# Kernel optimization log

Measured on AMD Instinct MI355X. Metric: run time of the kernel, lower is better.

## Reference

```python
import jax, jax.numpy as jnp
import numpy as np
from jax import lax

B, L = 4, 512
D_MODEL, D_STATE, D_CONV, EXPAND = 1024, 16, 4, 2
D_INNER = EXPAND * D_MODEL
DT_RANK = (D_MODEL + 15) // 16  # math.ceil(d_model / 16) = 64


def setup_inputs() -> dict:
    key = jax.random.key(0)
    ks = jax.random.split(key, 16)

    def rn(k, shape, scale=1.0):
        return jax.random.normal(k, shape, jnp.float32) * scale

    # A initialized as log(1..d_state) broadcast over d_inner, as in the module
    A_log = jnp.log(jnp.broadcast_to(jnp.arange(1, D_STATE + 1, dtype=jnp.float32), (D_INNER, D_STATE)))
    return {
        "hidden_states": rn(ks[0], (B, L, D_MODEL)),
        "in_proj_w": rn(ks[1], (2 * D_INNER, D_MODEL), D_MODEL ** -0.5),
        "conv1d_w": rn(ks[2], (D_INNER, 1, D_CONV), D_CONV ** -0.5),
        "conv1d_bias": rn(ks[3], (D_INNER,), 0.02),
        "x_proj_w": rn(ks[4], (DT_RANK + 2 * D_STATE, D_INNER), D_INNER ** -0.5),
        "dt_proj_w": rn(ks[5], (D_INNER, DT_RANK), DT_RANK ** -0.5),
        "dt_proj_bias": rn(ks[6], (D_INNER,), 0.02) - 4.0,
        "A_log": A_log,
        "D": jnp.ones((D_INNER,), jnp.float32),
        "conv1d_b_w": rn(ks[7], (D_INNER, 1, D_CONV), D_CONV ** -0.5),
        "conv1d_b_bias": rn(ks[8], (D_INNER,), 0.02),
        "x_proj_b_w": rn(ks[9], (DT_RANK + 2 * D_STATE, D_INNER), D_INNER ** -0.5),
        "dt_proj_b_w": rn(ks[10], (D_INNER, DT_RANK), DT_RANK ** -0.5),
        "dt_proj_b_bias": rn(ks[11], (D_INNER,), 0.02) - 4.0,
        "A_b_log": A_log,
        "D_b": jnp.ones((D_INNER,), jnp.float32),
        "out_proj_w": rn(ks[12], (D_MODEL, D_INNER), D_INNER ** -0.5),
    }


def _selective_scan(u, delta, A, Bm, Cm, Dv):
    # u, delta: [b,l,d]; Bm, Cm: [b,l,n]; A: [d,n]; Dv: [d]
    # h_t = exp(delta_t * A) * h_{t-1} + delta_t * B_t * u_t ; y_t = <h_t, C_t> + D * u_t
    def step(h, inp):
        u_t, dt_t, B_t, C_t = inp  # [b,d], [b,d], [b,n], [b,n]
        dA = jnp.exp(dt_t[:, :, None] * A)  # [b,d,n]
        h = dA * h + (dt_t * u_t)[:, :, None] * B_t[:, None, :]
        y = jnp.einsum('bdn,bn->bd', h, C_t)
        return h, y

    b, l, d = u.shape
    h0 = jnp.zeros((b, d, A.shape[1]), u.dtype)
    xs = (u.transpose(1, 0, 2), delta.transpose(1, 0, 2), Bm.transpose(1, 0, 2), Cm.transpose(1, 0, 2))
    _, ys = lax.scan(step, h0, xs)  # ys: [l,b,d]
    return ys.transpose(1, 0, 2) + u * Dv


def _direction(x_bdl, conv_w, conv_b, xproj_w, dtproj_w, dtproj_b, A_log, Dv):
    # x_bdl: [b, d_inner, l]. torch pads both sides with d_conv-1 then slices [:L] -> causal depthwise conv.
    xc = lax.conv_general_dilated(x_bdl, conv_w, (1,), [(D_CONV - 1, 0)],
                                  dimension_numbers=('NCH', 'OIH', 'NCH'),
                                  feature_group_count=D_INNER)
    xc = (xc + conv_b[None, :, None]).transpose(0, 2, 1)  # [b,l,d_inner]
    x_dbl = xc @ xproj_w.T  # [b,l,dt_rank+2n]
    dt = x_dbl[..., :DT_RANK] @ dtproj_w.T + dtproj_b
    Bm = x_dbl[..., DT_RANK:DT_RANK + D_STATE]
    Cm = x_dbl[..., DT_RANK + D_STATE:]
    xc = jnp.clip(xc, -10.0, 10.0)
    dt = jnp.clip(dt, 1e-5, 1.0)
    # source passes dt_proj.bias again as delta_bias with delta_softplus=True (bias added twice; faithful)
    delta = jax.nn.softplus(dt + dtproj_b)
    A = -jnp.exp(A_log)
    return _selective_scan(xc, delta, A, Bm, Cm, Dv)


def reference(hidden_states, in_proj_w, conv1d_w, conv1d_bias, x_proj_w, dt_proj_w, dt_proj_bias,
              A_log, D, conv1d_b_w, conv1d_b_bias, x_proj_b_w, dt_proj_b_w, dt_proj_b_bias,
              A_b_log, D_b, out_proj_w):
    xz = (hidden_states @ in_proj_w.T).transpose(0, 2, 1)  # [b, 2*d_inner, l]
    x, z = jnp.split(xz, 2, axis=1)  # each [b, d_inner, l]
    y_fwd = _direction(x, conv1d_w, conv1d_bias, x_proj_w, dt_proj_w, dt_proj_bias, A_log, D)
    y_bwd = _direction(x[:, :, ::-1], conv1d_b_w, conv1d_b_bias, x_proj_b_w, dt_proj_b_w,
                       dt_proj_b_bias, A_b_log, D_b)[:, ::-1, :]  # flip back along seq
    y = (y_fwd + y_bwd) * jax.nn.silu(z.transpose(0, 2, 1))  # [b,l,d_inner]
    out = y @ out_proj_w.T  # [b,l,d_model]
    return jnp.nan_to_num(out, nan=0.0, posinf=1.0, neginf=-1.0)
```

## Files before the change

### kernel.cpp

```cpp
#include <hip/hip_runtime.h>
#include <hip/hip_bf16.h>
#include <math.h>

#define BB 4
#define LL 512
#define DMODEL 1024
#define DSTATE 16
#define DCONV 4
#define DINNER 2048
#define DTRANK 64
#define MROWS (BB*LL)
#define G2KS 4
#define SCHUNK 32
#define SNC (LL / SCHUNK)

typedef __hip_bfloat16 bf16;
typedef __attribute__((ext_vector_type(8))) short short8;
typedef __attribute__((ext_vector_type(4))) short short4v;
typedef __attribute__((ext_vector_type(4))) float f32x4;

__device__ __forceinline__ float softplusf(float x) {
    return x > 20.f ? x : log1pf(__expf(x));
}

__device__ __forceinline__ void stage16(const void* g, void* l) {
    __builtin_amdgcn_global_load_lds(
        (const __attribute__((address_space(1))) void*)g,
        (__attribute__((address_space(3))) void*)l, 16, 0, 0);
}

__device__ __forceinline__ bool a_is_arange(const float* Aa) {
    bool ok = true;
#pragma unroll
    for (int n = 1; n < DSTATE; ++n) {
        float k = (float)(n + 1);
        ok = ok && (fabsf(Aa[n] - k * Aa[0]) <= 1e-4f * k * fabsf(Aa[0]));
    }
    return ok;
}

template<int EPI>
__global__ __launch_bounds__(256) void gemm_bf16(
    const bf16* __restrict__ A, const bf16* __restrict__ W,
    float* __restrict__ C, int N, int K, int lda, int ldw, int ldc)
{
    __shared__ bf16 lA[128 * 32];
    __shared__ bf16 lW[128 * 32];

    const int tid = threadIdx.x;
    const int lane = tid & 63;
    const int wid = tid >> 6;
    const int wr = wid >> 1;
    const int wc = wid & 1;
    const int rowBase = blockIdx.y * 128;
    const int colBase = blockIdx.x * 128;

    const int r16 = lane & 15;
    const int kg = lane >> 4;
    const int srow = (lane >> 2);
    const int scol = (lane & 3) * 8;

    f32x4 acc[4][4];
#pragma unroll
    for (int m = 0; m < 4; ++m)
#pragma unroll
        for (int n = 0; n < 4; ++n) acc[m][n] = (f32x4)0.f;

    for (int k0 = 0; k0 < K; k0 += 32) {
#pragma unroll
        for (int c = 0; c < 2; ++c) {
            int r = wid * 32 + c * 16 + srow;
            stage16(&A[(size_t)(rowBase + r) * lda + k0 + scol],
                    &lA[(wid * 32 + c * 16) * 32]);
            stage16(&W[(size_t)(colBase + r) * ldw + k0 + scol],
                    &lW[(wid * 32 + c * 16) * 32]);
        }
        __syncthreads();

        short8 a[4], b[4];
#pragma unroll
        for (int m = 0; m < 4; ++m)
            a[m] = *(const short8*)&lA[(wr * 64 + m * 16 + r16) * 32 + kg * 8];
#pragma unroll
        for (int n = 0; n < 4; ++n)
            b[n] = *(const short8*)&lW[(wc * 64 + n * 16 + r16) * 32 + kg * 8];
#pragma unroll
        for (int m = 0; m < 4; ++m)
#pragma unroll
            for (int n = 0; n < 4; ++n)
                acc[m][n] = __builtin_amdgcn_mfma_f32_16x16x32_bf16(
                    a[m], b[n], acc[m][n], 0, 0, 0);
        __syncthreads();
    }

#pragma unroll
    for (int m = 0; m < 4; ++m) {
#pragma unroll
        for (int n = 0; n < 4; ++n) {
            int gc = colBase + wc * 64 + n * 16 + r16;
#pragma unroll
            for (int j = 0; j < 4; ++j) {
                int gr = rowBase + wr * 64 + m * 16 + kg * 4 + j;
                float v = acc[m][n][j];
                if (EPI == 2) {
                    if (isnan(v)) v = 0.f;
                    else if (isinf(v)) v = (v > 0.f) ? 1.f : -1.f;
                }
                C[(size_t)gr * ldc + gc] = v;
            }
        }
    }
}

__global__ __launch_bounds__(256) void g4_mfma(
    const bf16* __restrict__ A, const bf16* __restrict__ W,
    float* __restrict__ part)
{
    const int kz = blockIdx.z;
    const int kOff = kz * 1024;
    float* C = part + (size_t)kz * 2048 * 1024;

    __shared__ bf16 lA[128 * 32];
    __shared__ bf16 lW[128 * 32];

    const int tid = threadIdx.x;
    const int lane = tid & 63;
    const int wid = tid >> 6;
    const int wr = wid >> 1;
    const int wc = wid & 1;
    const int rowBase = blockIdx.y * 128;
    const int colBase = blockIdx.x * 128;

    const int r16 = lane & 15;
    const int kg = lane >> 4;
    const int srow = (lane >> 2);
    const int scol = (lane & 3) * 8;

    f32x4 acc[4][4];
#pragma unroll
    for (int m = 0; m < 4; ++m)
#pragma unroll
        for (int n = 0; n < 4; ++n) acc[m][n] = (f32x4)0.f;

    for (int k0 = 0; k0 < 1024; k0 += 32) {
#pragma unroll
        for (int c = 0; c < 2; ++c) {
            int r = wid * 32 + c * 16 + srow;
            stage16(&A[(size_t)(rowBase + r) * 2048 + kOff + k0 + scol],
                    &lA[(wid * 32 + c * 16) * 32]);
            stage16(&W[(size_t)(colBase + r) * 2048 + kOff + k0 + scol],
                    &lW[(wid * 32 + c * 16) * 32]);
        }
        __syncthreads();

        short8 a[4], b[4];
#pragma unroll
        for (int m = 0; m < 4; ++m)
            a[m] = *(const short8*)&lA[(wr * 64 + m * 16 + r16) * 32 + kg * 8];
#pragma unroll
        for (int n = 0; n < 4; ++n)
            b[n] = *(const short8*)&lW[(wc * 64 + n * 16 + r16) * 32 + kg * 8];
#pragma unroll
        for (int m = 0; m < 4; ++m)
#pragma unroll
            for (int n = 0; n < 4; ++n)
                acc[m][n] = __builtin_amdgcn_mfma_f32_16x16x32_bf16(
                    a[m], b[n], acc[m][n], 0, 0, 0);
        __syncthreads();
    }

#pragma unroll
    for (int m = 0; m < 4; ++m) {
#pragma unroll
        for (int n = 0; n < 4; ++n) {
            int gc = colBase + wc * 64 + n * 16 + r16;
#pragma unroll
            for (int j = 0; j < 4; ++j) {
                int gr = rowBase + wr * 64 + m * 16 + kg * 4 + j;
                C[(size_t)gr * 1024 + gc] = acc[m][n][j];
            }
        }
    }
}

__global__ __launch_bounds__(256) void g4_reduce(
    const float* __restrict__ part, float* __restrict__ out)
{
    int i = (blockIdx.x * 256 + threadIdx.x) * 4;
    float4 p0 = *(const float4*)&part[i];
    float4 p1 = *(const float4*)&part[2048 * 1024 + i];
    float r[4] = { p0.x + p1.x, p0.y + p1.y, p0.z + p1.z, p0.w + p1.w };
#pragma unroll
    for (int j = 0; j < 4; ++j) {
        float v = r[j];
        if (isnan(v)) v = 0.f;
        else if (isinf(v)) v = (v > 0.f) ? 1.f : -1.f;
        r[j] = v;
    }
    *(float4*)&out[i] = *(float4*)r;
}

__global__ __launch_bounds__(256) void g3_mfma(
    const bf16* __restrict__ xdbl_bf,
    const bf16* __restrict__ dtw_bf,
    const float* __restrict__ biasf, const float* __restrict__ biasb,
    bf16* __restrict__ of, bf16* __restrict__ ob)
{
    const int dir = blockIdx.z;
    const bf16* A = xdbl_bf + (size_t)dir * 2048 * 96;
    const bf16* W = dtw_bf + (size_t)dir * 2048 * 64;
    const float* bias = dir ? biasb : biasf;
    bf16* C = dir ? ob : of;

    __shared__ bf16 lA[128 * 32];
    __shared__ bf16 lW[128 * 32];

    const int tid = threadIdx.x;
    const int lane = tid & 63;
    const int wid = tid >> 6;
    const int wr = wid >> 1;
    const int wc = wid & 1;
    const int rowBase = blockIdx.y * 128;
    const int colBase = blockIdx.x * 128;

    const int r16 = lane & 15;
    const int kg = lane >> 4;
    const int srow = (lane >> 2);
    const int scol = (lane & 3) * 8;

    f32x4 acc[4][4];
#pragma unroll
    for (int m = 0; m < 4; ++m)
#pragma unroll
        for (int n = 0; n < 4; ++n) acc[m][n] = (f32x4)0.f;

#pragma unroll
    for (int k0 = 0; k0 < 64; k0 += 32) {
#pragma unroll
        for (int c = 0; c < 2; ++c) {
            int r = wid * 32 + c * 16 + srow;
            stage16(&A[(size_t)(rowBase + r) * 96 + k0 + scol],
                    &lA[(wid * 32 + c * 16) * 32]);
            stage16(&W[(size_t)(colBase + r) * 64 + k0 + scol],
                    &lW[(wid * 32 + c * 16) * 32]);
        }
        __syncthreads();

        short8 a[4], b[4];
#pragma unroll
        for (int m = 0; m < 4; ++m)
            a[m] = *(const short8*)&lA[(wr * 64 + m * 16 + r16) * 32 + kg * 8];
#pragma unroll
        for (int n = 0; n < 4; ++n)
            b[n] = *(const short8*)&lW[(wc * 64 + n * 16 + r16) * 32 + kg * 8];
#pragma unroll
        for (int m = 0; m < 4; ++m)
#pragma unroll
            for (int n = 0; n < 4; ++n)
                acc[m][n] = __builtin_amdgcn_mfma_f32_16x16x32_bf16(
                    a[m], b[n], acc[m][n], 0, 0, 0);
        __syncthreads();
    }

#pragma unroll
    for (int m = 0; m < 4; ++m) {
#pragma unroll
        for (int n = 0; n < 4; ++n) {
            int gc = colBase + wc * 64 + n * 16 + r16;
            float bv = bias[gc];
#pragma unroll
            for (int j = 0; j < 4; ++j) {
                int gr = rowBase + wr * 64 + m * 16 + kg * 4 + j;
                float t = acc[m][n][j] + bv;
                t = fminf(fmaxf(t, 1e-5f), 1.0f);
                C[(size_t)gr * 2048 + gc] = __float2bfloat16(softplusf(t + bv));
            }
        }
    }
}

__global__ __launch_bounds__(256) void g2_mfma(
    const bf16* __restrict__ xcbf_f, const bf16* __restrict__ xcbf_b,
    const bf16* __restrict__ wxf, const bf16* __restrict__ wxb,
    float* __restrict__ part)
{
    const int dir = blockIdx.z;
    const bf16* A = dir ? xcbf_b : xcbf_f;
    const bf16* W = dir ? wxb : wxf;
    const int rowBase = blockIdx.x * 128;
    const int kz = blockIdx.y;
    const int kBase = kz * (2048 / G2KS);

    __shared__ bf16 lA[128 * 40];
    __shared__ bf16 lW[96 * 40];

    const int tid = threadIdx.x;
    const int lane = tid & 63;
    const int wid = tid >> 6;
    const int r16 = lane & 15;
    const int kg = lane >> 4;

    f32x4 acc[2][6];
#pragma unroll
    for (int m = 0; m < 2; ++m)
#pragma unroll
        for (int n = 0; n < 6; ++n) acc[m][n] = (f32x4)0.f;

    const int srow = tid >> 2;
    const int scol = (tid & 3) * 8;

    for (int k0 = 0; k0 < 2048 / G2KS; k0 += 32) {
#pragma unroll
        for (int it = 0; it < 2; ++it) {
            int r = srow + it * 64;
            short8 va = *(const short8*)&A[(size_t)(rowBase + r) * 2048 + kBase + k0 + scol];
            *(short8*)&lA[r * 40 + scol] = va;
        }
        {
            short8 vw = *(const short8*)&W[(size_t)srow * 2048 + kBase + k0 + scol];
            *(short8*)&lW[srow * 40 + scol] = vw;
        }
        if (tid < 128) {
            int r = 64 + (tid >> 2);
            short8 vw2 = *(const short8*)&W[(size_t)r * 2048 + kBase + k0 + scol];
            *(short8*)&lW[r * 40 + scol] = vw2;
        }
        __syncthreads();

        short8 a[2], b[6];
#pragma unroll
        for (int m = 0; m < 2; ++m)
            a[m] = *(const short8*)&lA[(wid * 32 + m * 16 + r16) * 40 + kg * 8];
#pragma unroll
        for (int n = 0; n < 6; ++n)
            b[n] = *(const short8*)&lW[(n * 16 + r16) * 40 + kg * 8];
#pragma unroll
        for (int m = 0; m < 2; ++m)
#pragma unroll
            for (int n = 0; n < 6; ++n)
                acc[m][n] = __builtin_amdgcn_mfma_f32_16x16x32_bf16(
                    a[m], b[n], acc[m][n], 0, 0, 0);
        __syncthreads();
    }

    float* p = part + ((size_t)(dir * G2KS + kz) * 2048) * 96;
#pragma unroll
    for (int m = 0; m < 2; ++m) {
#pragma unroll
        for (int n = 0; n < 6; ++n) {
            int gc = n * 16 + r16;
#pragma unroll
            for (int j = 0; j < 4; ++j) {
                int gr = rowBase + wid * 32 + m * 16 + kg * 4 + j;
                p[(size_t)gr * 96 + gc] = acc[m][n][j];
            }
        }
    }
}

__global__ __launch_bounds__(256) void g2_reduce(
    const float* __restrict__ part, float* __restrict__ xf, float* __restrict__ xb,
    bf16* __restrict__ xdbl_bf)
{
    int idx = blockIdx.x * 256 + threadIdx.x;
    int c = idx % 96;
    int r = (idx / 96) & 2047;
    int dir = idx / (96 * 2048);
    float s = 0.f;
#pragma unroll
    for (int ks = 0; ks < G2KS; ++ks)
        s += part[((size_t)(dir * G2KS + ks) * 2048 + r) * 96 + c];
    (dir ? xb : xf)[(size_t)r * 96 + c] = s;
    xdbl_bf[((size_t)dir * 2048 + r) * 96 + c] = __float2bfloat16(s);
}

__global__ __launch_bounds__(256) void cast_all(
    const float* __restrict__ hidden, const float* __restrict__ in_proj_w,
    const float* __restrict__ xproj_w, const float* __restrict__ xproj_bw,
    const float* __restrict__ dtproj_w, const float* __restrict__ dtproj_bw,
    bf16* __restrict__ hbf, bf16* __restrict__ wbf,
    bf16* __restrict__ wxf, bf16* __restrict__ wxb,
    bf16* __restrict__ dtwf, bf16* __restrict__ dtwb)
{
    int bid = blockIdx.x;
    const float* src; bf16* dst; int base;
    if (bid < 1024)      { src = hidden;    dst = hbf;  base = bid; }
    else if (bid < 3072) { src = in_proj_w; dst = wbf;  base = bid - 1024; }
    else if (bid < 3168) { src = xproj_w;   dst = wxf;  base = bid - 3072; }
    else if (bid < 3264) { src = xproj_bw;  dst = wxb;  base = bid - 3168; }
    else if (bid < 3328) { src = dtproj_w;  dst = dtwf; base = bid - 3264; }
    else                 { src = dtproj_bw; dst = dtwb; base = bid - 3328; }
    int i = (base * 256 + threadIdx.x) * 8;
    float4 x = *(const float4*)&src[i];
    float4 y = *(const float4*)&src[i + 4];
    bf16 t[8] = { __float2bfloat16(x.x), __float2bfloat16(x.y),
                  __float2bfloat16(x.z), __float2bfloat16(x.w),
                  __float2bfloat16(y.x), __float2bfloat16(y.y),
                  __float2bfloat16(y.z), __float2bfloat16(y.w) };
    *(short8*)&dst[i] = *(short8*)t;
}

__global__ __launch_bounds__(256) void conv_kernel(
    const float* __restrict__ xz,
    const float* __restrict__ wf, const float* __restrict__ bf,
    const float* __restrict__ wb, const float* __restrict__ bb,
    bf16* __restrict__ xcbf, bf16* __restrict__ xcbb)
{
    int idx = blockIdx.x * 256 + threadIdx.x;
    int dg = idx & 511;
    int rest = idx >> 9;
    int l = rest & (LL - 1);
    int b = (rest >> 9) & (BB - 1);
    int dir = rest >> 11;
    int d0 = dg * 4;

    const float* w = dir ? wb : wf;
    const float* bias = dir ? bb : bf;

    float4 wv[4];
#pragma unroll
    for (int c = 0; c < 4; ++c)
        wv[c] = *(const float4*)&w[(d0 + c) * DCONV];

    float4 acc = *(const float4*)&bias[d0];
#pragma unroll
    for (int k = 0; k < DCONV; ++k) {
        int j = l - (DCONV - 1) + k;
        if (j >= 0) {
            int jj = dir ? (LL - 1 - j) : j;
            float4 x = *(const float4*)&xz[((size_t)(b * LL + jj)) * (2 * DINNER) + d0];
            acc.x += ((const float*)&wv[0])[k] * x.x;
            acc.y += ((const float*)&wv[1])[k] * x.y;
            acc.z += ((const float*)&wv[2])[k] * x.z;
            acc.w += ((const float*)&wv[3])[k] * x.w;
        }
    }

    size_t off = ((size_t)(b * LL + l)) * DINNER + d0;
    bf16 t[4] = { __float2bfloat16(acc.x), __float2bfloat16(acc.y),
                  __float2bfloat16(acc.z), __float2bfloat16(acc.w) };
    *(short4v*)&((dir ? xcbb : xcbf)[off]) = *(short4v*)t;
}

__global__ __launch_bounds__(256) void scan1_kernel(
    const float* __restrict__ Alog_f, const float* __restrict__ Alog_b,
    const float* __restrict__ xdbl_f, const float* __restrict__ xdbl_b,
    const bf16* __restrict__ xc_f, const bf16* __restrict__ xc_b,
    const bf16* __restrict__ dl_f, const bf16* __restrict__ dl_b,
    float* __restrict__ sdel, float* __restrict__ hend)
{
    const int tid = threadIdx.x;
    const int d = blockIdx.x * 256 + tid;
    const int c = blockIdx.y;
    const int z = blockIdx.z;
    const int dir = z >> 2, b = z & 3;

    const float* Alog = dir ? Alog_b : Alog_f;
    const float* xdbl = dir ? xdbl_b : xdbl_f;
    const bf16* xc    = dir ? xc_b   : xc_f;
    const bf16* dl    = dir ? dl_b   : dl_f;
    const int rowBase = b * LL + c * SCHUNK;

    __shared__ float bs[SCHUNK][16];
#pragma unroll
    for (int i = 0; i < SCHUNK * 16 / 256; ++i) {
        int e = tid + 256 * i;
        int r = e >> 4, n = e & 15;
        bs[r][n] = xdbl[(size_t)(rowBase + r) * 96 + DTRANK + n];
    }
    __syncthreads();

    float Aa[DSTATE], h[DSTATE];
#pragma unroll
    for (int n = 0; n < DSTATE; ++n) {
        Aa[n] = -__expf(Alog[d * DSTATE + n]);
        h[n] = 0.f;
    }
    float sd = 0.f;
    const bool fast = a_is_arange(Aa);
    const float a0l2 = Aa[0] * 1.44269504f;

    float nxd = __bfloat162float(dl[(size_t)rowBase * DINNER + d]);
    float nxu = __bfloat162float(xc[(size_t)rowBase * DINNER + d]);

    if (fast) {
#pragma unroll 4
        for (int t = 0; t < SCHUNK; ++t) {
            float delta = nxd, u = nxu;
            if (t + 1 < SCHUNK) {
                size_t nrow = (size_t)(rowBase + t + 1);
                nxd = __bfloat162float(dl[nrow * DINNER + d]);
                nxu = __bfloat162float(xc[nrow * DINNER + d]);
            }
            u = fminf(fmaxf(u, -10.f), 10.f);
            float du = delta * u;
            sd += delta;
            float p[DSTATE];
            p[0] = exp2f(delta * a0l2);
#pragma unroll
            for (int n = 1; n < DSTATE; ++n)
                p[n] = p[n >> 1] * p[(n - 1) >> 1];
#pragma unroll
            for (int n = 0; n < DSTATE; ++n)
                h[n] = p[n] * h[n] + du * bs[t][n];
        }
    } else {
#pragma unroll 4
        for (int t = 0; t < SCHUNK; ++t) {
            float delta = nxd, u = nxu;
            if (t + 1 < SCHUNK) {
                size_t nrow = (size_t)(rowBase + t + 1);
                nxd = __bfloat162float(dl[nrow * DINNER + d]);
                nxu = __bfloat162float(xc[nrow * DINNER + d]);
            }
            u = fminf(fmaxf(u, -10.f), 10.f);
            float du = delta * u;
            sd += delta;
#pragma unroll
            for (int n = 0; n < DSTATE; ++n)
                h[n] = __expf(delta * Aa[n]) * h[n] + du * bs[t][n];
        }
    }

    size_t base = (size_t)z * SNC + c;
    sdel[base * DINNER + d] = sd;
#pragma unroll
    for (int n = 0; n < DSTATE; ++n)
        hend[(base * DSTATE + n) * DINNER + d] = h[n];
}

__global__ __launch_bounds__(256) void scan_combine(
    const float* __restrict__ Alog_f, const float* __restrict__ Alog_b,
    const float* __restrict__ sdel, float* __restrict__ hend)
{
    int g = blockIdx.x * 256 + threadIdx.x;
    int d = g & (DINNER - 1);
    int n = (g >> 11) & (DSTATE - 1);
    int z = g >> 15;
    const float* Alog = (z >> 2) ? Alog_b : Alog_f;

    float Aa = -__expf(Alog[d * DSTATE + n]);
    float hr = 0.f;
    for (int c = 0; c < SNC; ++c) {
        size_t base = (size_t)z * SNC + c;
        size_t idx = (base * DSTATE + n) * DINNER + d;
        float he = hend[idx];
        hend[idx] = hr;
        float sd = sdel[base * DINNER + d];
        hr = __expf(sd * Aa) * hr + he;
    }
}

__global__ __launch_bounds__(256) void scan2_kernel(
    const float* __restrict__ Alog_f, const float* __restrict__ Alog_b,
    const float* __restrict__ Df, const float* __restrict__ Db,
    const float* __restrict__ xdbl_f, const float* __restrict__ xdbl_b,
    const bf16* __restrict__ xc_f, const bf16* __restrict__ xc_b,
    const float* __restrict__ hin,
    bf16* __restrict__ dl_f, bf16* __restrict__ dl_b)
{
    const int tid = threadIdx.x;
    const int d = blockIdx.x * 256 + tid;
    const int c = blockIdx.y;
    const int z = blockIdx.z;
    const int dir = z >> 2, b = z & 3;

    const float* Alog = dir ? Alog_b : Alog_f;
    const float* xdbl = dir ? xdbl_b : xdbl_f;
    const bf16* xc    = dir ? xc_b   : xc_f;
    bf16* dl          = dir ? dl_b   : dl_f;
    const int rowBase = b * LL + c * SCHUNK;

    __shared__ float bs[SCHUNK][32];
#pragma unroll
    for (int i = 0; i < SCHUNK * 32 / 256; ++i) {
        int e = tid + 256 * i;
        int r = e >> 5, n = e & 31;
        bs[r][n] = xdbl[(size_t)(rowBase + r) * 96 + DTRANK + n];
    }
    __syncthreads();

    float Dv = (dir ? Db : Df)[d];
    size_t base = (size_t)z * SNC + c;
    float Aa[DSTATE], h[DSTATE];
#pragma unroll
    for (int n = 0; n < DSTATE; ++n) {
        Aa[n] = -__expf(Alog[d * DSTATE + n]);
        h[n] = hin[(base * DSTATE + n) * DINNER + d];
    }
    const bool fast = a_is_arange(Aa);
    const float a0l2 = Aa[0] * 1.44269504f;

    float nxd = __bfloat162float(dl[(size_t)rowBase * DINNER + d]);
    float nxu = __bfloat162float(xc[(size_t)rowBase * DINNER + d]);

    if (fast) {
#pragma unroll 4
        for (int t = 0; t < SCHUNK; ++t) {
            float delta = nxd, u = nxu;
            if (t + 1 < SCHUNK) {
                size_t nrow = (size_t)(rowBase + t + 1);
                nxd = __bfloat162float(dl[nrow * DINNER + d]);
                nxu = __bfloat162float(xc[nrow * DINNER + d]);
            }
            u = fminf(fmaxf(u, -10.f), 10.f);
            float du = delta * u;
            float p[DSTATE];
            p[0] = exp2f(delta * a0l2);
#pragma unroll
            for (int n = 1; n < DSTATE; ++n)
                p[n] = p[n >> 1] * p[(n - 1) >> 1];
            float y = 0.f;
#pragma unroll
            for (int n = 0; n < DSTATE; ++n) {
                h[n] = p[n] * h[n] + du * bs[t][n];
                y += h[n] * bs[t][DSTATE + n];
            }
            dl[(size_t)(rowBase + t) * DINNER + d] = __float2bfloat16(y + u * Dv);
        }
    } else {
#pragma unroll 4
        for (int t = 0; t < SCHUNK; ++t) {
            float delta = nxd, u = nxu;
            if (t + 1 < SCHUNK) {
                size_t nrow = (size_t)(rowBase + t + 1);
                nxd = __bfloat162float(dl[nrow * DINNER + d]);
                nxu = __bfloat162float(xc[nrow * DINNER + d]);
            }
            u = fminf(fmaxf(u, -10.f), 10.f);
            float du = delta * u;
            float y = 0.f;
#pragma unroll
            for (int n = 0; n < DSTATE; ++n) {
                h[n] = __expf(delta * Aa[n]) * h[n] + du * bs[t][n];
                y += h[n] * bs[t][DSTATE + n];
            }
            dl[(size_t)(rowBase + t) * DINNER + d] = __float2bfloat16(y + u * Dv);
        }
    }
}

__global__ __launch_bounds__(256) void gate_cast(
    const bf16* __restrict__ yf, const bf16* __restrict__ yb,
    const float* __restrict__ xz, bf16* __restrict__ ytot,
    const float* __restrict__ out_pw, bf16* __restrict__ obf)
{
    int bid = blockIdx.x;
    if (bid < 16384) {
        int idx = bid * 256 + threadIdx.x;
        int d = idx & (DINNER - 1);
        int l = (idx >> 11) & (LL - 1);
        int b = idx >> 20;
        size_t rowf = (size_t)(b * LL + l);
        size_t rowb = (size_t)(b * LL + (LL - 1 - l));
        float y = __bfloat162float(yf[rowf * DINNER + d]) +
                  __bfloat162float(yb[rowb * DINNER + d]);
        float z = xz[rowf * (2 * DINNER) + DINNER + d];
        float s = z / (1.f + __expf(-z));
        ytot[rowf * DINNER + d] = __float2bfloat16(y * s);
    } else {
        int i = ((bid - 16384) * 256 + threadIdx.x) * 8;
        float4 x = *(const float4*)&out_pw[i];
        float4 y = *(const float4*)&out_pw[i + 4];
        bf16 t[8] = { __float2bfloat16(x.x), __float2bfloat16(x.y),
                      __float2bfloat16(x.z), __float2bfloat16(x.w),
                      __float2bfloat16(y.x), __float2bfloat16(y.y),
                      __float2bfloat16(y.z), __float2bfloat16(y.w) };
        *(short8*)&obf[i] = *(short8*)t;
    }
}

extern "C" void kernel_launch(void* const* d_in, const int* in_sizes, int n_in,
                              void* d_out, int out_size, void* d_ws, size_t ws_size,
                              hipStream_t stream)
{
    const float* hidden    = (const float*)d_in[0];
    const float* in_proj_w = (const float*)d_in[1];
    const float* conv_w    = (const float*)d_in[2];
    const float* conv_b    = (const float*)d_in[3];
    const float* xproj_w   = (const float*)d_in[4];
    const float* dtproj_w  = (const float*)d_in[5];
    const float* dtproj_b  = (const float*)d_in[6];
    const float* A_log     = (const float*)d_in[7];
    const float* Dvec      = (const float*)d_in[8];
    const float* conv_bw   = (const float*)d_in[9];
    const float* conv_bb   = (const float*)d_in[10];
    const float* xproj_bw  = (const float*)d_in[11];
    const float* dtproj_bw = (const float*)d_in[12];
    const float* dtproj_bb = (const float*)d_in[13];
    const float* A_b_log   = (const float*)d_in[14];
    const float* D_b       = (const float*)d_in[15];
    const float* out_pw    = (const float*)d_in[16];
    float* out = (float*)d_out;

    float* ws = (float*)d_ws;
    float* xz      = ws;
    float* xcR_f   = xz + 8388608;
    float* xcR_b   = xcR_f + 4194304;
    float* xdbl_f  = xcR_b + 4194304;
    float* xdbl_b  = xdbl_f + 196608;
    float* dlR_f   = xdbl_b + 196608;
    float* dlR_b   = dlR_f + 4194304;
    float* g2part  = dlR_b + 4194304;
    float* sdel    = g2part + 1572864;
    float* hend    = sdel + 262144;
    float* smallb  = hend + 4194304;

    bf16* xcbf = (bf16*)xcR_f;
    bf16* xcbb = (bf16*)xcR_b;
    bf16* dlbf_f = (bf16*)dlR_f;
    bf16* dlbf_b = (bf16*)dlR_b;
    bf16* hbf = (bf16*)dlR_f;
    bf16* wbf = (bf16*)(dlR_f + 1048576);
    bf16* wxf = (bf16*)dlR_b;
    bf16* wxb = (bf16*)(dlR_b + 98304);
    bf16* xdbl_bf = (bf16*)smallb;
    bf16* dtw_bf  = (bf16*)(smallb + 196608);
    bf16* ytot_bf = (bf16*)xcR_f;
    bf16* obf = (bf16*)xcR_b;
    float* g4part = dlR_f;

    dim3 blk(256);

    cast_all<<<dim3(3392), blk, 0, stream>>>(
        hidden, in_proj_w, xproj_w, xproj_bw, dtproj_w, dtproj_bw,
        hbf, wbf, wxf, wxb, dtw_bf, dtw_bf + 131072);

    gemm_bf16<0><<<dim3(4096 / 128, MROWS / 128), blk, 0, stream>>>(
        hbf, wbf, xz, 4096, 1024, 1024, 1024, 4096);

    conv_kernel<<<dim3(2 * BB * LL * DINNER / 4 / 256), blk, 0, stream>>>(
        xz, conv_w, conv_b, conv_bw, conv_bb, xcbf, xcbb);

    g2_mfma<<<dim3(16, G2KS, 2), blk, 0, stream>>>(
        xcbf, xcbb, wxf, wxb, g2part);
    g2_reduce<<<dim3(2 * 2048 * 96 / 256), blk, 0, stream>>>(
        g2part, xdbl_f, xdbl_b, xdbl_bf);

    g3_mfma<<<dim3(16, 16, 2), blk, 0, stream>>>(
        xdbl_bf, dtw_bf, dtproj_b, dtproj_bb, dlbf_f, dlbf_b);

    scan1_kernel<<<dim3(DINNER / 256, SNC, 8), blk, 0, stream>>>(
        A_log, A_b_log, xdbl_f, xdbl_b, xcbf, xcbb, dlbf_f, dlbf_b, sdel, hend);
    scan_combine<<<dim3(2 * BB * DSTATE * DINNER / 256), blk, 0, stream>>>(
        A_log, A_b_log, sdel, hend);
    scan2_kernel<<<dim3(DINNER / 256, SNC, 8), blk, 0, stream>>>(
        A_log, A_b_log, Dvec, D_b, xdbl_f, xdbl_b, xcbf, xcbb, hend, dlbf_f, dlbf_b);

    gate_cast<<<dim3(16384 + 1024), blk, 0, stream>>>(
        dlbf_f, dlbf_b, xz, ytot_bf, out_pw, obf);

    g4_mfma<<<dim3(1024 / 128, MROWS / 128, 2), blk, 0, stream>>>(
        ytot_bf, obf, g4part);
    g4_reduce<<<dim3(2048 * 1024 / 4 / 256), blk, 0, stream>>>(g4part, out);
}
```

Measured before the change: 219.3 us.

## Store in_proj output as bf16 and stage 64-wide K slices in GEMMs

The in_proj GEMM now writes xz as bf16 instead of fp32, and conv and gate kernels read bf16. This halves the traffic of the largest intermediate. Separately, the three MFMA GEMMs load two 32-wide K slices per barrier pair, halving the number of __syncthreads per K step at the cost of doubled LDS usage. The bf16 xz adds rounding error to the conv input and gate z values.

```diff
diff --git a/kernel.cpp b/kernel.cpp
--- a/kernel.cpp
+++ b/kernel.cpp
@@ -39,13 +39,12 @@
     return ok;
 }
 
-template<int EPI>
 __global__ __launch_bounds__(256) void gemm_bf16(
     const bf16* __restrict__ A, const bf16* __restrict__ W,
-    float* __restrict__ C, int N, int K, int lda, int ldw, int ldc)
-{
-    __shared__ bf16 lA[128 * 32];
-    __shared__ bf16 lW[128 * 32];
+    bf16* __restrict__ C, int N, int K, int lda, int ldw, int ldc)
+{
+    __shared__ bf16 lA[2][128 * 32];
+    __shared__ bf16 lW[2][128 * 32];
 
     const int tid = threadIdx.x;
     const int lane = tid & 63;
@@ -66,30 +65,36 @@
 #pragma unroll
         for (int n = 0; n < 4; ++n) acc[m][n] = (f32x4)0.f;
 
-    for (int k0 = 0; k0 < K; k0 += 32) {
-#pragma unroll
-        for (int c = 0; c < 2; ++c) {
-            int r = wid * 32 + c * 16 + srow;
-            stage16(&A[(size_t)(rowBase + r) * lda + k0 + scol],
-                    &lA[(wid * 32 + c * 16) * 32]);
-            stage16(&W[(size_t)(colBase + r) * ldw + k0 + scol],
-                    &lW[(wid * 32 + c * 16) * 32]);
+    for (int k0 = 0; k0 < K; k0 += 64) {
+#pragma unroll
+        for (int h = 0; h < 2; ++h) {
+#pragma unroll
+            for (int c = 0; c < 2; ++c) {
+                int r = wid * 32 + c * 16 + srow;
+                stage16(&A[(size_t)(rowBase + r) * lda + k0 + h * 32 + scol],
+                        &lA[h][(wid * 32 + c * 16) * 32]);
+                stage16(&W[(size_t)(colBase + r) * ldw + k0 + h * 32 + scol],
+                        &lW[h][(wid * 32 + c * 16) * 32]);
+            }
         }
         __syncthreads();
 
-        short8 a[4], b[4];
-#pragma unroll
-        for (int m = 0; m < 4; ++m)
-            a[m] = *(const short8*)&lA[(wr * 64 + m * 16 + r16) * 32 + kg * 8];
-#pragma unroll
-        for (int n = 0; n < 4; ++n)
-            b[n] = *(const short8*)&lW[(wc * 64 + n * 16 + r16) * 32 + kg * 8];
-#pragma unroll
-        for (int m = 0; m < 4; ++m)
+#pragma unroll
+        for (int h = 0; h < 2; ++h) {
+            short8 a[4], b[4];
+#pragma unroll
+            for (int m = 0; m < 4; ++m)
+                a[m] = *(const short8*)&lA[h][(wr * 64 + m * 16 + r16) * 32 + kg * 8];
 #pragma unroll
             for (int n = 0; n < 4; ++n)
-                acc[m][n] = __builtin_amdgcn_mfma_f32_16x16x32_bf16(
-                    a[m], b[n], acc[m][n], 0, 0, 0);
+                b[n] = *(const short8*)&lW[h][(wc * 64 + n * 16 + r16) * 32 + kg * 8];
+#pragma unroll
+            for (int m = 0; m < 4; ++m)
+#pragma unroll
+                for (int n = 0; n < 4; ++n)
+                    acc[m][n] = __builtin_amdgcn_mfma_f32_16x16x32_bf16(
+                        a[m], b[n], acc[m][n], 0, 0, 0);
+        }
         __syncthreads();
     }
 
@@ -101,12 +106,7 @@
 #pragma unroll
             for (int j = 0; j < 4; ++j) {
                 int gr = rowBase + wr * 64 + m * 16 + kg * 4 + j;
-                float v = acc[m][n][j];
-                if (EPI == 2) {
-                    if (isnan(v)) v = 0.f;
-                    else if (isinf(v)) v = (v > 0.f) ? 1.f : -1.f;
-                }
-                C[(size_t)gr * ldc + gc] = v;
+                C[(size_t)gr * ldc + gc] = __float2bfloat16(acc[m][n][j]);
             }
         }
     }
@@ -120,8 +120,8 @@
     const int kOff = kz * 1024;
     float* C = part + (size_t)kz * 2048 * 1024;
 
-    __shared__ bf16 lA[128 * 32];
-    __shared__ bf16 lW[128 * 32];
+    __shared__ bf16 lA[2][128 * 32];
+    __shared__ bf16 lW[2][128 * 32];
 
     const int tid = threadIdx.x;
     const int lane = tid & 63;
@@ -142,30 +142,36 @@
 #pragma unroll
         for (int n = 0; n < 4; ++n) acc[m][n] = (f32x4)0.f;
 
-    for (int k0 = 0; k0 < 1024; k0 += 32) {
-#pragma unroll
-        for (int c = 0; c < 2; ++c) {
-            int r = wid * 32 + c * 16 + srow;
-            stage16(&A[(size_t)(rowBase + r) * 2048 + kOff + k0 + scol],
-                    &lA[(wid * 32 + c * 16) * 32]);
-            stage16(&W[(size_t)(colBase + r) * 2048 + kOff + k0 + scol],
-                    &lW[(wid * 32 + c * 16) * 32]);
+    for (int k0 = 0; k0 < 1024; k0 += 64) {
+#pragma unroll
+        for (int h = 0; h < 2; ++h) {
+#pragma unroll
+            for (int c = 0; c < 2; ++c) {
+                int r = wid * 32 + c * 16 + srow;
+                stage16(&A[(size_t)(rowBase + r) * 2048 + kOff + k0 + h * 32 + scol],
+                        &lA[h][(wid * 32 + c * 16) * 32]);
+                stage16(&W[(size_t)(colBase + r) * 2048 + kOff + k0 + h * 32 + scol],
+                        &lW[h][(wid * 32 + c * 16) * 32]);
+            }
         }
         __syncthreads();
 
-        short8 a[4], b[4];
-#pragma unroll
-        for (int m = 0; m < 4; ++m)
-            a[m] = *(const short8*)&lA[(wr * 64 + m * 16 + r16) * 32 + kg * 8];
-#pragma unroll
-        for (int n = 0; n < 4; ++n)
-            b[n] = *(const short8*)&lW[(wc * 64 + n * 16 + r16) * 32 + kg * 8];
-#pragma unroll
-        for (int m = 0; m < 4; ++m)
+#pragma unroll
+        for (int h = 0; h < 2; ++h) {
+            short8 a[4], b[4];
+#pragma unroll
+            for (int m = 0; m < 4; ++m)
+                a[m] = *(const short8*)&lA[h][(wr * 64 + m * 16 + r16) * 32 + kg * 8];
 #pragma unroll
             for (int n = 0; n < 4; ++n)
-                acc[m][n] = __builtin_amdgcn_mfma_f32_16x16x32_bf16(
-                    a[m], b[n], acc[m][n], 0, 0, 0);
+                b[n] = *(const short8*)&lW[h][(wc * 64 + n * 16 + r16) * 32 + kg * 8];
+#pragma unroll
+            for (int m = 0; m < 4; ++m)
+#pragma unroll
+                for (int n = 0; n < 4; ++n)
+                    acc[m][n] = __builtin_amdgcn_mfma_f32_16x16x32_bf16(
+                        a[m], b[n], acc[m][n], 0, 0, 0);
+        }
         __syncthreads();
     }
 
@@ -212,8 +218,8 @@
     const float* bias = dir ? biasb : biasf;
     bf16* C = dir ? ob : of;
 
-    __shared__ bf16 lA[128 * 32];
-    __shared__ bf16 lW[128 * 32];
+    __shared__ bf16 lA[2][128 * 32];
+    __shared__ bf16 lW[2][128 * 32];
 
     const int tid = threadIdx.x;
     const int lane = tid & 63;
@@ -235,31 +241,33 @@
         for (int n = 0; n < 4; ++n) acc[m][n] = (f32x4)0.f;
 
 #pragma unroll
-    for (int k0 = 0; k0 < 64; k0 += 32) {
+    for (int h = 0; h < 2; ++h) {
 #pragma unroll
         for (int c = 0; c < 2; ++c) {
             int r = wid * 32 + c * 16 + srow;
-            stage16(&A[(size_t)(rowBase + r) * 96 + k0 + scol],
-                    &lA[(wid * 32 + c * 16) * 32]);
-            stage16(&W[(size_t)(colBase + r) * 64 + k0 + scol],
-                    &lW[(wid * 32 + c * 16) * 32]);
-        }
-        __syncthreads();
-
+            stage16(&A[(size_t)(rowBase + r) * 96 + h * 32 + scol],
+                    &lA[h][(wid * 32 + c * 16) * 32]);
+            stage16(&W[(size_t)(colBase + r) * 64 + h * 32 + scol],
+                    &lW[h][(wid * 32 + c * 16) * 32]);
+        }
+    }
+    __syncthreads();
+
+#pragma unroll
+    for (int h = 0; h < 2; ++h) {
         short8 a[4], b[4];
 #pragma unroll
         for (int m = 0; m < 4; ++m)
-            a[m] = *(const short8*)&lA[(wr * 64 + m * 16 + r16) * 32 + kg * 8];
+            a[m] = *(const short8*)&lA[h][(wr * 64 + m * 16 + r16) * 32 + kg * 8];
 #pragma unroll
         for (int n = 0; n < 4; ++n)
-            b[n] = *(const short8*)&lW[(wc * 64 + n * 16 + r16) * 32 + kg * 8];
+            b[n] = *(const short8*)&lW[h][(wc * 64 + n * 16 + r16) * 32 + kg * 8];
 #pragma unroll
         for (int m = 0; m < 4; ++m)
 #pragma unroll
             for (int n = 0; n < 4; ++n)
                 acc[m][n] = __builtin_amdgcn_mfma_f32_16x16x32_bf16(
                     a[m], b[n], acc[m][n], 0, 0, 0);
-        __syncthreads();
     }
 
 #pragma unroll
@@ -401,7 +409,7 @@
 }
 
 __global__ __launch_bounds__(256) void conv_kernel(
-    const float* __restrict__ xz,
+    const bf16* __restrict__ xz,
     const float* __restrict__ wf, const float* __restrict__ bf,
     const float* __restrict__ wb, const float* __restrict__ bb,
     bf16* __restrict__ xcbf, bf16* __restrict__ xcbb)
@@ -428,11 +436,12 @@
         int j = l - (DCONV - 1) + k;
         if (j >= 0) {
             int jj = dir ? (LL - 1 - j) : j;
-            float4 x = *(const float4*)&xz[((size_t)(b * LL + jj)) * (2 * DINNER) + d0];
-            acc.x += ((const float*)&wv[0])[k] * x.x;
-            acc.y += ((const float*)&wv[1])[k] * x.y;
-            acc.z += ((const float*)&wv[2])[k] * x.z;
-            acc.w += ((const float*)&wv[3])[k] * x.w;
+            short4v xv = *(const short4v*)&xz[((size_t)(b * LL + jj)) * (2 * DINNER) + d0];
+            const bf16* xp = (const bf16*)&xv;
+            acc.x += ((const float*)&wv[0])[k] * __bfloat162float(xp[0]);
+            acc.y += ((const float*)&wv[1])[k] * __bfloat162float(xp[1]);
+            acc.z += ((const float*)&wv[2])[k] * __bfloat162float(xp[2]);
+            acc.w += ((const float*)&wv[3])[k] * __bfloat162float(xp[3]);
         }
     }
 
@@ -642,7 +651,7 @@
 
 __global__ __launch_bounds__(256) void gate_cast(
     const bf16* __restrict__ yf, const bf16* __restrict__ yb,
-    const float* __restrict__ xz, bf16* __restrict__ ytot,
+    const bf16* __restrict__ xz, bf16* __restrict__ ytot,
     const float* __restrict__ out_pw, bf16* __restrict__ obf)
 {
     int bid = blockIdx.x;
@@ -655,7 +664,7 @@
         size_t rowb = (size_t)(b * LL + (LL - 1 - l));
         float y = __bfloat162float(yf[rowf * DINNER + d]) +
                   __bfloat162float(yb[rowb * DINNER + d]);
-        float z = xz[rowf * (2 * DINNER) + DINNER + d];
+        float z = __bfloat162float(xz[rowf * (2 * DINNER) + DINNER + d]);
         float s = z / (1.f + __expf(-z));
         ytot[rowf * DINNER + d] = __float2bfloat16(y * s);
     } else {
@@ -694,8 +703,8 @@
     float* out = (float*)d_out;
 
     float* ws = (float*)d_ws;
-    float* xz      = ws;
-    float* xcR_f   = xz + 8388608;
+    float* xzR     = ws;
+    float* xcR_f   = xzR + 8388608;
     float* xcR_b   = xcR_f + 4194304;
     float* xdbl_f  = xcR_b + 4194304;
     float* xdbl_b  = xdbl_f + 196608;
@@ -706,6 +715,7 @@
     float* hend    = sdel + 262144;
     float* smallb  = hend + 4194304;
 
+    bf16* xzbf = (bf16*)xzR;
     bf16* xcbf = (bf16*)xcR_f;
     bf16* xcbb = (bf16*)xcR_b;
     bf16* dlbf_f = (bf16*)dlR_f;
@@ -726,11 +736,11 @@
         hidden, in_proj_w, xproj_w, xproj_bw, dtproj_w, dtproj_bw,
         hbf, wbf, wxf, wxb, dtw_bf, dtw_bf + 131072);
 
-    gemm_bf16<0><<<dim3(4096 / 128, MROWS / 128), blk, 0, stream>>>(
-        hbf, wbf, xz, 4096, 1024, 1024, 1024, 4096);
+    gemm_bf16<<<dim3(4096 / 128, MROWS / 128), blk, 0, stream>>>(
+        hbf, wbf, xzbf, 4096, 1024, 1024, 1024, 4096);
 
     conv_kernel<<<dim3(2 * BB * LL * DINNER / 4 / 256), blk, 0, stream>>>(
-        xz, conv_w, conv_b, conv_bw, conv_bb, xcbf, xcbb);
+        xzbf, conv_w, conv_b, conv_bw, conv_bb, xcbf, xcbb);
 
     g2_mfma<<<dim3(16, G2KS, 2), blk, 0, stream>>>(
         xcbf, xcbb, wxf, wxb, g2part);
@@ -748,7 +758,7 @@
         A_log, A_b_log, Dvec, D_b, xdbl_f, xdbl_b, xcbf, xcbb, hend, dlbf_f, dlbf_b);
 
     gate_cast<<<dim3(16384 + 1024), blk, 0, stream>>>(
-        dlbf_f, dlbf_b, xz, ytot_bf, out_pw, obf);
+        dlbf_f, dlbf_b, xzbf, ytot_bf, out_pw, obf);
 
     g4_mfma<<<dim3(1024 / 128, MROWS / 128, 2), blk, 0, stream>>>(
         ytot_bf, obf, g4part);
```

Measured after the change: 212.0 us (median of 5 runs). -3.3%, faster.
